# Performance work log

Hardware: AMD Instinct MI355X
Metric: run time of the kernel (lower is better)

## Reference

```python
import jax, jax.numpy as jnp
import numpy as np

D_MODEL = 512
D_STATE = 64
SEQ_LEN = 8192
BATCH = 8
LN_EPS = 1e-3  # keras LayerNormalization default epsilon
DELTA_MIN = 0.001
DELTA_MAX = 0.8 * (2.0 / D_STATE)  # default when use_hippo_init=True


def setup_inputs() -> dict:
    key = jax.random.key(0)
    ks = jax.random.split(key, 10)
    x = jax.random.normal(ks[0], (BATCH, SEQ_LEN, D_MODEL), dtype=jnp.float32)
    # Dense layers: glorot-uniform-ish init via scaled normal for simplicity
    def dense_w(k, fan_in, fan_out):
        lim = np.sqrt(6.0 / (fan_in + fan_out))
        return jax.random.uniform(k, (fan_in, fan_out), minval=-lim, maxval=lim, dtype=jnp.float32)
    W_in = dense_w(ks[1], D_MODEL, D_MODEL)
    b_in = jnp.zeros((D_MODEL,), jnp.float32)
    W_xs = dense_w(ks[2], D_MODEL, D_STATE)
    # HiPPO-LegS log init: A_log = log(n+1)
    A_log = jnp.log(jnp.arange(1, D_STATE + 1, dtype=jnp.float32))
    log_delta = jax.random.uniform(ks[3], (D_STATE,), minval=np.log(DELTA_MIN), maxval=np.log(DELTA_MAX), dtype=jnp.float32)
    B = jnp.ones((D_STATE,), jnp.float32)
    C = jax.random.normal(ks[4], (D_STATE,), dtype=jnp.float32)  # stddev=1.0
    D = jnp.ones((D_MODEL,), jnp.float32)
    W_so = dense_w(ks[5], D_STATE, D_MODEL)
    W_out = dense_w(ks[6], D_MODEL, D_MODEL)
    b_out = jnp.zeros((D_MODEL,), jnp.float32)
    ln_gamma = jnp.ones((D_MODEL,), jnp.float32)
    ln_beta = jnp.zeros((D_MODEL,), jnp.float32)
    return {
        "x": x, "ln_gamma": ln_gamma, "ln_beta": ln_beta,
        "W_in": W_in, "b_in": b_in, "W_xs": W_xs,
        "A_log": A_log, "log_delta": log_delta, "B": B, "C": C, "D": D,
        "W_so": W_so, "W_out": W_out, "b_out": b_out,
    }


def reference(x, ln_gamma, ln_beta, W_in, b_in, W_xs, A_log, log_delta, B, C, D, W_so, W_out, b_out):
    Bsz, L, dm = x.shape
    n_fft = 1 << int(np.ceil(np.log2(2 * L - 1)))
    residual = x
    # LayerNorm over last axis (keras default)
    mu = jnp.mean(x, axis=-1, keepdims=True)
    var = jnp.mean(jnp.square(x - mu), axis=-1, keepdims=True)
    xn = (x - mu) * jax.lax.rsqrt(var + LN_EPS) * ln_gamma + ln_beta
    z = xn @ W_in + b_in                       # (B, L, d_model)
    x_state = z @ W_xs                          # (B, L, d_state)
    # Diagonal SSM discretization (bilinear/Tustin)
    A = -jnp.exp(A_log)
    delta = jax.nn.softplus(log_delta)
    dA2 = delta * A / 2.0
    A_bar = (1.0 + dA2) / (1.0 - dA2)           # (d_state,)
    B_bar = delta / (1.0 - dA2) * B             # (d_state,)
    t = jnp.arange(L, dtype=jnp.float32)
    kernel = jnp.power(A_bar[None, :], t[:, None]) * B_bar[None, :]  # (L, d_state)
    # FFT convolution along time
    u_t = jnp.transpose(x_state, (0, 2, 1))     # (B, d_state, L)
    k_t = kernel.T                              # (d_state, L)
    u_f = jnp.fft.rfft(u_t, n=n_fft, axis=-1)
    k_f = jnp.fft.rfft(k_t, n=n_fft, axis=-1)
    y = jnp.fft.irfft(u_f * k_f[None, :, :], n=n_fft, axis=-1)[:, :, :L]
    y_state = jnp.transpose(y, (0, 2, 1))       # (B, L, d_state)
    y_state = y_state * C[None, None, :]
    y = y_state @ W_so                          # (B, L, d_model)
    y = y + D * z
    y = y @ W_out + b_out
    return y + residual
```

## Files before the change

### kernel.cpp

```cpp
#include <hip/hip_runtime.h>
#include <hip/hip_bf16.h>
#include <cstddef>
#include <cstdint>

#define DM 512
#define DS 64
#define L_SEQ 8192
#define NB 8
#define M_ROWS (NB * L_SEQ)
#define LN_EPS 1e-3f
#define NCHUNK 256
#define LCH 32

typedef __attribute__((ext_vector_type(8))) short short8;
typedef __attribute__((ext_vector_type(4))) float f32x4;
using bf16 = __hip_bfloat16;
using ushort_t = unsigned short;

__device__ __forceinline__ unsigned short f2bf(float f) {
    bf16 h = __float2bfloat16(f);
    return *reinterpret_cast<unsigned short*>(&h);
}

__device__ __forceinline__ int swzcol(int row, int col) {
    return (col & ~63) | (((((col >> 3) & 7) ^ (row & 7))) << 3) | (col & 7);
}

__device__ __forceinline__ size_t pkidx(int k, int n, int Kd32) {
    int n16 = n >> 4, fr = n & 15, kt = k >> 5, fq = (k >> 3) & 3, e = k & 7;
    return (((size_t)(n16 * Kd32 + kt) * 64 + fq * 16 + fr) << 3) + e;
}

__device__ __forceinline__ void gload_lds16(const void* g, void* l) {
    __builtin_amdgcn_global_load_lds(
        (const __attribute__((address_space(1))) void*)g,
        (__attribute__((address_space(3))) void*)l, 16, 0, 0);
}

template<int N> __device__ __forceinline__ void wait_vm() {
    static_assert(N == 0 || N == 2, "");
    if constexpr (N == 0) asm volatile("s_waitcnt vmcnt(0)" ::: "memory");
    else                  asm volatile("s_waitcnt vmcnt(2)" ::: "memory");
}

__device__ __forceinline__ void block_barrier() {
    asm volatile("" ::: "memory");
    __builtin_amdgcn_s_barrier();
    asm volatile("" ::: "memory");
}

__global__ __launch_bounds__(256) void prep(const float* __restrict__ W_so,
                                            const float* __restrict__ W_out,
                                            const float* __restrict__ W_in,
                                            const float* __restrict__ W_xs,
                                            const float* __restrict__ b_in,
                                            const float* __restrict__ b_out,
                                            const float* __restrict__ Dv,
                                            float* __restrict__ sWc2,
                                            float* __restrict__ sWc1,
                                            float* __restrict__ bc1,
                                            float* __restrict__ sWc3,
                                            float* __restrict__ bc2)
{
    int i = blockIdx.x * 256 + threadIdx.x;
    if (i < 32768) {
        int s = i >> 9, j = i & 511;
        float a = 0.f;
        for (int c = 0; c < 512; ++c) a += W_so[s * 512 + c] * W_out[c * 512 + j];
        sWc2[i] = a;
    } else if (i < 65536) {
        int idx = i - 32768; int k = idx >> 6, n = idx & 63;
        float a = 0.f;
        for (int c = 0; c < 512; ++c) a += W_in[k * 512 + c] * W_xs[c * 64 + n];
        sWc1[idx] = a;
    } else if (i < 65600) {
        int n = i - 65536;
        float a = 0.f;
        for (int c = 0; c < 512; ++c) a += b_in[c] * W_xs[c * 64 + n];
        bc1[n] = a;
    } else if (i < 327744) {
        int idx = i - 65600; int k = idx >> 9, j = idx & 511;
        float a = 0.f;
        for (int c = 0; c < 512; ++c) a += W_in[k * 512 + c] * Dv[c] * W_out[c * 512 + j];
        sWc3[idx] = a;
    } else if (i < 328256) {
        int j = i - 327744;
        float a = b_out[j];
        for (int c = 0; c < 512; ++c) a += b_in[c] * Dv[c] * W_out[c * 512 + j];
        bc2[j] = a;
    }
}

__global__ __launch_bounds__(256) void pack_all(const float* __restrict__ sWc3,
                                                const float* __restrict__ sWc1,
                                                const float* __restrict__ sWc2,
                                                ushort_t* __restrict__ Wc3Pk,
                                                ushort_t* __restrict__ Wc1Pk,
                                                ushort_t* __restrict__ Wc2Pk)
{
    int i = blockIdx.x * 256 + threadIdx.x;
    if (i < 262144) {
        int k = i >> 9, n = i & 511;
        Wc3Pk[pkidx(k, n, 16)] = f2bf(sWc3[i]);
    } else if (i < 294912) {
        int j = i - 262144; int k = j >> 6, n = j & 63;
        Wc1Pk[pkidx(k, n, 16)] = f2bf(sWc1[j]);
    } else if (i < 327680) {
        int j = i - 294912; int s = j >> 9, n = j & 511;
        Wc2Pk[pkidx(s, n, 2)] = f2bf(sWc2[j]);
    }
}

__global__ __launch_bounds__(256) void ln_xs(const float* __restrict__ x,
                                             const float* __restrict__ gamma,
                                             const float* __restrict__ beta,
                                             const ushort_t* __restrict__ Wc1Pk,
                                             const float* __restrict__ bc1,
                                             ushort_t* __restrict__ xn,
                                             float* __restrict__ xs)
{
    __shared__ ushort_t xt[16 * 512];
    const int tid = threadIdx.x;
    const int lane = tid & 63, w = tid >> 6;
    const int fr = lane & 15, fq = lane >> 4;
    const size_t row0 = (size_t)blockIdx.x * 16;

    const float4* g4 = (const float4*)gamma;
    const float4* b4 = (const float4*)beta;
    float4 g0 = g4[lane * 2], g1 = g4[lane * 2 + 1];
    float4 bb0 = b4[lane * 2], bb1 = b4[lane * 2 + 1];

    #pragma unroll
    for (int rr = 0; rr < 4; ++rr) {
        int r = w * 4 + rr;
        size_t row = row0 + r;
        const float4* xr = (const float4*)(x + row * DM);
        float4 v0 = xr[lane * 2], v1 = xr[lane * 2 + 1];
        float s  = v0.x + v0.y + v0.z + v0.w + v1.x + v1.y + v1.z + v1.w;
        float s2 = v0.x*v0.x + v0.y*v0.y + v0.z*v0.z + v0.w*v0.w
                 + v1.x*v1.x + v1.y*v1.y + v1.z*v1.z + v1.w*v1.w;
        #pragma unroll
        for (int off = 32; off > 0; off >>= 1) {
            s  += __shfl_xor(s,  off);
            s2 += __shfl_xor(s2, off);
        }
        float mu  = s * (1.0f / DM);
        float var = s2 * (1.0f / DM) - mu * mu;
        float rs  = rsqrtf(var + LN_EPS);
        short8 o;
        o[0] = (short)f2bf((v0.x - mu) * rs * g0.x + bb0.x);
        o[1] = (short)f2bf((v0.y - mu) * rs * g0.y + bb0.y);
        o[2] = (short)f2bf((v0.z - mu) * rs * g0.z + bb0.z);
        o[3] = (short)f2bf((v0.w - mu) * rs * g0.w + bb0.w);
        o[4] = (short)f2bf((v1.x - mu) * rs * g1.x + bb1.x);
        o[5] = (short)f2bf((v1.y - mu) * rs * g1.y + bb1.y);
        o[6] = (short)f2bf((v1.z - mu) * rs * g1.z + bb1.z);
        o[7] = (short)f2bf((v1.w - mu) * rs * g1.w + bb1.w);
        int g = (lane & 7) ^ ((int)row & 7);
        *(short8*)(xn + row * DM + (lane >> 3) * 64 + g * 8) = o;
        *(short8*)&xt[r * 512 + (lane >> 3) * 64 + g * 8] = o;
    }
    __syncthreads();

    f32x4 acc = (f32x4){0.f, 0.f, 0.f, 0.f};
    #pragma unroll
    for (int kt = 0; kt < 16; ++kt) {
        int seg = kt >> 1;
        int gk = ((kt & 1) * 4 + fq) ^ (fr & 7);
        short8 af = *(const short8*)&xt[fr * 512 + seg * 64 + gk * 8];
        short8 bf = *(const short8*)(Wc1Pk + (((size_t)(w * 16 + kt) * 64 + lane) << 3));
        acc = __builtin_amdgcn_mfma_f32_16x16x32_bf16(af, bf, acc, 0, 0, 0);
    }
    float bv = bc1[w * 16 + fr];
    #pragma unroll
    for (int r2 = 0; r2 < 4; ++r2)
        xs[(row0 + fq * 4 + r2) * DS + w * 16 + fr] = acc[r2] + bv;
}

__device__ __forceinline__ void store_out(float* C, size_t i, float v) { C[i] = v; }
__device__ __forceinline__ void store_out(bf16* C, size_t i, float v)  { C[i] = __float2bfloat16(v); }

template<int BN, int WR, int WC, typename OutT, bool DUAL, bool HB, bool HA, bool SWZO>
__global__ __launch_bounds__(512, 4) void gemm_bp(const ushort_t* __restrict__ A1,
                                                  const ushort_t* __restrict__ B1,
                                                  const ushort_t* __restrict__ A2,
                                                  const ushort_t* __restrict__ B2,
                                                  const float* __restrict__ bias,
                                                  const float* __restrict__ aux,
                                                  OutT* __restrict__ C,
                                                  int M, int N, int K2)
{
    constexpr int BM = 128;
    constexpr int MF = BM / (16 * WR), NF = BN / (16 * WC);
    static_assert(NF == 2, "b ping-pong arrays assume NF==2");
    __shared__ unsigned char LDS[3][BM * 128];

    const int tid = threadIdx.x;
    const int lane = tid & 63, w = tid >> 6;
    const int fr = lane & 15, fq = lane >> 4;
    const int wr = w % WR, wc = w / WR;

    const int ny = N / BN;
    const int per = (int)gridDim.x >> 3;
    const int lg = ((int)blockIdx.x & 7) * per + ((int)blockIdx.x >> 3);
    const size_t bm0 = (size_t)(lg / ny) * BM;
    const int bn0 = (lg % ny) * BN;
    const int nk = (DUAL ? 1 : 0) + K2 / 64;

    f32x4 acc[MF][NF];
    #pragma unroll
    for (int m = 0; m < MF; ++m)
        #pragma unroll
        for (int n = 0; n < NF; ++n)
            acc[m][n] = (f32x4){0.f, 0.f, 0.f, 0.f};

    auto stage = [&](int buf, int t) {
        #pragma unroll
        for (int j = 0; j < 2; ++j) {
            int r = j * 64 + (tid >> 3);
            const ushort_t* src;
            if constexpr (DUAL) {
                if (t == 0) src = A1 + (bm0 + r) * (size_t)64 + (tid & 7) * 8;
                else        src = A2 + (bm0 + r) * (size_t)512 + (size_t)(t - 1) * 64 + (tid & 7) * 8;
            } else {
                src = A2 + (bm0 + r) * (size_t)K2 + (size_t)t * 64 + (tid & 7) * 8;
            }
            gload_lds16(src, &LDS[buf][j * 8192 + w * 1024]);
        }
    };

    auto loadB = [&](short8 (&bb)[2][2], int t) {
        #pragma unroll
        for (int h = 0; h < 2; ++h)
            #pragma unroll
            for (int n = 0; n < NF; ++n) {
                int n16g = (bn0 + wc * (BN / WC) + n * 16) >> 4;
                const ushort_t* p;
                if constexpr (DUAL) {
                    if (t == 0) p = B1 + (((size_t)(n16g * 2 + h) * 64 + lane) << 3);
                    else        p = B2 + (((size_t)(n16g * 16 + (t - 1) * 2 + h) * 64 + lane) << 3);
                } else {
                    p = B2 + (((size_t)(n16g * (K2 / 32) + t * 2 + h) * 64 + lane) << 3);
                }
                bb[h][n] = *(const short8*)p;
            }
    };

    auto compute = [&](int buf, const short8 (&bb)[2][2]) {
        #pragma unroll
        for (int h = 0; h < 2; ++h) {
            short8 af[MF];
            #pragma unroll
            for (int m = 0; m < MF; ++m) {
                int row = wr * (BM / WR) + m * 16 + fr;
                int g = (h * 4 + fq) ^ (row & 7);
                af[m] = *(const short8*)&LDS[buf][row * 128 + g * 16];
            }
            #pragma unroll
            for (int m = 0; m < MF; ++m)
                #pragma unroll
                for (int n = 0; n < NF; ++n)
                    acc[m][n] = __builtin_amdgcn_mfma_f32_16x16x32_bf16(af[m], bb[h][n], acc[m][n], 0, 0, 0);
        }
    };

    short8 bX[2][2], bY[2][2];
    stage(0, 0);
    loadB(bX, 0);
    if (nk > 1) stage(1, 1);

    #define PHASE(T, BCUR, BNEXT)                                            \
        do {                                                                 \
            if ((T) + 1 < nk) wait_vm<2>(); else wait_vm<0>();               \
            block_barrier();                                                 \
            if ((T) + 1 < nk) loadB(BNEXT, (T) + 1);                         \
            if ((T) + 2 < nk) stage(((T) + 2) % 3, (T) + 2);                 \
            __builtin_amdgcn_sched_barrier(0);                               \
            compute((T) % 3, BCUR);                                          \
        } while (0)

    for (int t = 0; t < nk; t += 2) {
        PHASE(t, bX, bY);
        if (t + 1 < nk) PHASE(t + 1, bY, bX);
    }
    #undef PHASE

    #pragma unroll
    for (int n = 0; n < NF; ++n) {
        int coll = wc * (BN / WC) + n * 16 + fr;
        int colg = bn0 + coll;
        float bv = HB ? bias[colg] : 0.f;
        #pragma unroll
        for (int m = 0; m < MF; ++m) {
            int rowl = wr * (BM / WR) + m * 16 + fq * 4;
            #pragma unroll
            for (int r = 0; r < 4; ++r) {
                size_t row = bm0 + rowl + r;
                float v = acc[m][n][r] + bv;
                if constexpr (HA) v += aux[row * (size_t)N + colg];
                size_t oc = SWZO ? (size_t)swzcol(rowl + r, colg) : (size_t)colg;
                store_out(C, row * (size_t)N + oc, v);
            }
        }
    }
}

__device__ __forceinline__ void ssm_params(const float* A_log, const float* log_delta,
                                           const float* Bv, int n, float& Ab, float& Bb)
{
    float A  = -expf(A_log[n]);
    float dl = log1pf(expf(log_delta[n]));
    float dA2 = dl * A * 0.5f;
    float inv = 1.0f / (1.0f - dA2);
    Ab = (1.0f + dA2) * inv;
    Bb = dl * inv * Bv[n];
}

__global__ __launch_bounds__(64) void scan_pass1(const float* __restrict__ xs,
                                                 const float* __restrict__ A_log,
                                                 const float* __restrict__ log_delta,
                                                 const float* __restrict__ Bv,
                                                 float* __restrict__ carry)
{
    int b = blockIdx.x / NCHUNK;
    int c = blockIdx.x % NCHUNK;
    int n = threadIdx.x;
    float Ab, Bb;
    ssm_params(A_log, log_delta, Bv, n, Ab, Bb);
    size_t base = ((size_t)b * L_SEQ + (size_t)c * LCH) * DS + n;
    float h = 0.0f;
    for (int t = 0; t < LCH; ++t)
        h = Ab * h + Bb * xs[base + (size_t)t * DS];
    carry[((size_t)b * NCHUNK + c) * DS + n] = h;
}

__global__ __launch_bounds__(64) void scan_pass2(const float* __restrict__ A_log,
                                                 const float* __restrict__ log_delta,
                                                 const float* __restrict__ Bv,
                                                 const float* __restrict__ carry,
                                                 float* __restrict__ hin)
{
    int b = blockIdx.x;
    int n = threadIdx.x;
    float Ab, Bb;
    ssm_params(A_log, log_delta, Bv, n, Ab, Bb);
    float powA = powf(Ab, (float)LCH);
    float h = 0.0f;
    for (int c = 0; c < NCHUNK; ++c) {
        size_t idx = ((size_t)b * NCHUNK + c) * DS + n;
        hin[idx] = h;
        h = powA * h + carry[idx];
    }
}

__global__ __launch_bounds__(64) void scan_pass3(const float* __restrict__ xs,
                                                 const float* __restrict__ A_log,
                                                 const float* __restrict__ log_delta,
                                                 const float* __restrict__ Bv,
                                                 const float* __restrict__ Cv,
                                                 const float* __restrict__ hin,
                                                 ushort_t* __restrict__ ys)
{
    int b = blockIdx.x / NCHUNK;
    int c = blockIdx.x % NCHUNK;
    int n = threadIdx.x;
    float Ab, Bb;
    ssm_params(A_log, log_delta, Bv, n, Ab, Bb);
    float Cn = Cv[n];
    size_t base = ((size_t)b * L_SEQ + (size_t)c * LCH) * DS + n;
    size_t rowbase = ((size_t)b * L_SEQ + (size_t)c * LCH) * DS;
    float h = hin[((size_t)b * NCHUNK + c) * DS + n];
    for (int t = 0; t < LCH; ++t) {
        h = Ab * h + Bb * xs[base + (size_t)t * DS];
        int col = (((n >> 3) ^ (t & 7)) << 3) | (n & 7);
        ys[rowbase + (size_t)t * DS + col] = f2bf(Cn * h);
    }
}

extern "C" void kernel_launch(void* const* d_in, const int* in_sizes, int n_in,
                              void* d_out, int out_size, void* d_ws, size_t ws_size,
                              hipStream_t stream)
{
    const float* x         = (const float*)d_in[0];
    const float* ln_gamma  = (const float*)d_in[1];
    const float* ln_beta   = (const float*)d_in[2];
    const float* W_in      = (const float*)d_in[3];
    const float* b_in      = (const float*)d_in[4];
    const float* W_xs      = (const float*)d_in[5];
    const float* A_log     = (const float*)d_in[6];
    const float* log_delta = (const float*)d_in[7];
    const float* Bv        = (const float*)d_in[8];
    const float* Cv        = (const float*)d_in[9];
    const float* Dv        = (const float*)d_in[10];
    const float* W_so      = (const float*)d_in[11];
    const float* W_out     = (const float*)d_in[12];
    const float* b_out     = (const float*)d_in[13];
    float* out = (float*)d_out;

    const size_t M = M_ROWS;
    float*    xs_f   = (float*)d_ws;
    ushort_t* xn_b   = (ushort_t*)(xs_f + M * DS);
    ushort_t* ys_b   = xn_b + M * (size_t)DM;
    ushort_t* Wc3Pk  = ys_b + M * (size_t)DS;
    ushort_t* Wc1Pk  = Wc3Pk + (size_t)DM * DM;
    ushort_t* Wc2Pk  = Wc1Pk + (size_t)DM * DS;
    float*    sWc2   = (float*)(Wc2Pk + (size_t)DS * DM);
    float*    sWc1   = sWc2 + (size_t)DS * DM;
    float*    bc1    = sWc1 + (size_t)DM * DS;
    float*    sWc3   = bc1 + 64;
    float*    bc2    = sWc3 + (size_t)DM * DM;
    float*    carry  = bc2 + DM;
    float*    hin    = carry + NB * NCHUNK * DS;

    prep<<<dim3(1283), dim3(256), 0, stream>>>(W_so, W_out, W_in, W_xs, b_in, b_out, Dv,
                                               sWc2, sWc1, bc1, sWc3, bc2);
    pack_all<<<dim3(1280), dim3(256), 0, stream>>>(sWc3, sWc1, sWc2, Wc3Pk, Wc1Pk, Wc2Pk);
    ln_xs<<<dim3((unsigned)(M / 16)), dim3(256), 0, stream>>>(x, ln_gamma, ln_beta,
                                                              Wc1Pk, bc1, xn_b, xs_f);
    scan_pass1<<<dim3(NB * NCHUNK), dim3(64), 0, stream>>>(xs_f, A_log, log_delta, Bv, carry);
    scan_pass2<<<dim3(NB), dim3(64), 0, stream>>>(A_log, log_delta, Bv, carry, hin);
    scan_pass3<<<dim3(NB * NCHUNK), dim3(64), 0, stream>>>(xs_f, A_log, log_delta, Bv, Cv, hin, ys_b);
    gemm_bp<128, 2, 4, float, true, true, true, false>
        <<<dim3((M / 128) * (DM / 128)), dim3(512), 0, stream>>>(ys_b, Wc2Pk, xn_b, Wc3Pk,
                                                                 bc2, x, out, (int)M, DM, DM);
}
```

Baseline: 214.1 us.

## Fuse weight prep/pack, merge scan passes, replace final GEMM with full-row block kernel

Weight folding and bf16 packing now happen in a single kernel that writes packed weights directly, with no fp32 staging arrays. The sequential carry pass is removed: each chunk block recomputes its incoming state by looping over preceding chunk carries. The pipelined tiled dual GEMM is replaced by a kernel where each block loads a 64-row slab of xn into LDS once and eight waves each cover 64 output columns, with B fragments read directly from global. This cuts launches but adds redundant carry work (quadratic in chunk count) and drops the triple-buffered pipelining of the old GEMM.

After: 327.8 us. +53.1%, slower.

```diff
diff --git a/kernel.cpp b/kernel.cpp
--- a/kernel.cpp
+++ b/kernel.cpp
@@ -22,10 +22,6 @@
     return *reinterpret_cast<unsigned short*>(&h);
 }
 
-__device__ __forceinline__ int swzcol(int row, int col) {
-    return (col & ~63) | (((((col >> 3) & 7) ^ (row & 7))) << 3) | (col & 7);
-}
-
 __device__ __forceinline__ size_t pkidx(int k, int n, int Kd32) {
     int n16 = n >> 4, fr = n & 15, kt = k >> 5, fq = (k >> 3) & 3, e = k & 7;
     return (((size_t)(n16 * Kd32 + kt) * 64 + fq * 16 + fr) << 3) + e;
@@ -37,77 +33,45 @@
         (__attribute__((address_space(3))) void*)l, 16, 0, 0);
 }
 
-template<int N> __device__ __forceinline__ void wait_vm() {
-    static_assert(N == 0 || N == 2, "");
-    if constexpr (N == 0) asm volatile("s_waitcnt vmcnt(0)" ::: "memory");
-    else                  asm volatile("s_waitcnt vmcnt(2)" ::: "memory");
-}
-
-__device__ __forceinline__ void block_barrier() {
-    asm volatile("" ::: "memory");
-    __builtin_amdgcn_s_barrier();
-    asm volatile("" ::: "memory");
-}
-
-__global__ __launch_bounds__(256) void prep(const float* __restrict__ W_so,
-                                            const float* __restrict__ W_out,
-                                            const float* __restrict__ W_in,
-                                            const float* __restrict__ W_xs,
-                                            const float* __restrict__ b_in,
-                                            const float* __restrict__ b_out,
-                                            const float* __restrict__ Dv,
-                                            float* __restrict__ sWc2,
-                                            float* __restrict__ sWc1,
-                                            float* __restrict__ bc1,
-                                            float* __restrict__ sWc3,
-                                            float* __restrict__ bc2)
+__global__ __launch_bounds__(256) void wprep(const float* __restrict__ W_so,
+                                             const float* __restrict__ W_out,
+                                             const float* __restrict__ W_in,
+                                             const float* __restrict__ W_xs,
+                                             const float* __restrict__ b_in,
+                                             const float* __restrict__ b_out,
+                                             const float* __restrict__ Dv,
+                                             ushort_t* __restrict__ Wc3Pk,
+                                             ushort_t* __restrict__ Wc1Pk,
+                                             ushort_t* __restrict__ Wc2Pk,
+                                             float* __restrict__ bc1,
+                                             float* __restrict__ bc2)
 {
     int i = blockIdx.x * 256 + threadIdx.x;
-    if (i < 32768) {
-        int s = i >> 9, j = i & 511;
+    if (i < 262144) {
+        int k = i >> 9, n = i & 511;
         float a = 0.f;
-        for (int c = 0; c < 512; ++c) a += W_so[s * 512 + c] * W_out[c * 512 + j];
-        sWc2[i] = a;
-    } else if (i < 65536) {
-        int idx = i - 32768; int k = idx >> 6, n = idx & 63;
+        for (int c = 0; c < 512; ++c) a += W_in[k * 512 + c] * Dv[c] * W_out[c * 512 + n];
+        Wc3Pk[pkidx(k, n, 16)] = f2bf(a);
+    } else if (i < 294912) {
+        int j = i - 262144; int k = j >> 6, n = j & 63;
         float a = 0.f;
         for (int c = 0; c < 512; ++c) a += W_in[k * 512 + c] * W_xs[c * 64 + n];
-        sWc1[idx] = a;
-    } else if (i < 65600) {
-        int n = i - 65536;
+        Wc1Pk[pkidx(k, n, 16)] = f2bf(a);
+    } else if (i < 327680) {
+        int j = i - 294912; int s = j >> 9, n = j & 511;
+        float a = 0.f;
+        for (int c = 0; c < 512; ++c) a += W_so[s * 512 + c] * W_out[c * 512 + n];
+        Wc2Pk[pkidx(s, n, 2)] = f2bf(a);
+    } else if (i < 328192) {
+        int n = i - 327680;
+        float a = b_out[n];
+        for (int c = 0; c < 512; ++c) a += b_in[c] * Dv[c] * W_out[c * 512 + n];
+        bc2[n] = a;
+    } else if (i < 328256) {
+        int n = i - 328192;
         float a = 0.f;
         for (int c = 0; c < 512; ++c) a += b_in[c] * W_xs[c * 64 + n];
         bc1[n] = a;
-    } else if (i < 327744) {
-        int idx = i - 65600; int k = idx >> 9, j = idx & 511;
-        float a = 0.f;
-        for (int c = 0; c < 512; ++c) a += W_in[k * 512 + c] * Dv[c] * W_out[c * 512 + j];
-        sWc3[idx] = a;
-    } else if (i < 328256) {
-        int j = i - 327744;
-        float a = b_out[j];
-        for (int c = 0; c < 512; ++c) a += b_in[c] * Dv[c] * W_out[c * 512 + j];
-        bc2[j] = a;
-    }
-}
-
-__global__ __launch_bounds__(256) void pack_all(const float* __restrict__ sWc3,
-                                                const float* __restrict__ sWc1,
-                                                const float* __restrict__ sWc2,
-                                                ushort_t* __restrict__ Wc3Pk,
-                                                ushort_t* __restrict__ Wc1Pk,
-                                                ushort_t* __restrict__ Wc2Pk)
-{
-    int i = blockIdx.x * 256 + threadIdx.x;
-    if (i < 262144) {
-        int k = i >> 9, n = i & 511;
-        Wc3Pk[pkidx(k, n, 16)] = f2bf(sWc3[i]);
-    } else if (i < 294912) {
-        int j = i - 262144; int k = j >> 6, n = j & 63;
-        Wc1Pk[pkidx(k, n, 16)] = f2bf(sWc1[j]);
-    } else if (i < 327680) {
-        int j = i - 294912; int s = j >> 9, n = j & 511;
-        Wc2Pk[pkidx(s, n, 2)] = f2bf(sWc2[j]);
     }
 }
 
@@ -177,134 +141,6 @@
         xs[(row0 + fq * 4 + r2) * DS + w * 16 + fr] = acc[r2] + bv;
 }
 
-__device__ __forceinline__ void store_out(float* C, size_t i, float v) { C[i] = v; }
-__device__ __forceinline__ void store_out(bf16* C, size_t i, float v)  { C[i] = __float2bfloat16(v); }
-
-template<int BN, int WR, int WC, typename OutT, bool DUAL, bool HB, bool HA, bool SWZO>
-__global__ __launch_bounds__(512, 4) void gemm_bp(const ushort_t* __restrict__ A1,
-                                                  const ushort_t* __restrict__ B1,
-                                                  const ushort_t* __restrict__ A2,
-                                                  const ushort_t* __restrict__ B2,
-                                                  const float* __restrict__ bias,
-                                                  const float* __restrict__ aux,
-                                                  OutT* __restrict__ C,
-                                                  int M, int N, int K2)
-{
-    constexpr int BM = 128;
-    constexpr int MF = BM / (16 * WR), NF = BN / (16 * WC);
-    static_assert(NF == 2, "b ping-pong arrays assume NF==2");
-    __shared__ unsigned char LDS[3][BM * 128];
-
-    const int tid = threadIdx.x;
-    const int lane = tid & 63, w = tid >> 6;
-    const int fr = lane & 15, fq = lane >> 4;
-    const int wr = w % WR, wc = w / WR;
-
-    const int ny = N / BN;
-    const int per = (int)gridDim.x >> 3;
-    const int lg = ((int)blockIdx.x & 7) * per + ((int)blockIdx.x >> 3);
-    const size_t bm0 = (size_t)(lg / ny) * BM;
-    const int bn0 = (lg % ny) * BN;
-    const int nk = (DUAL ? 1 : 0) + K2 / 64;
-
-    f32x4 acc[MF][NF];
-    #pragma unroll
-    for (int m = 0; m < MF; ++m)
-        #pragma unroll
-        for (int n = 0; n < NF; ++n)
-            acc[m][n] = (f32x4){0.f, 0.f, 0.f, 0.f};
-
-    auto stage = [&](int buf, int t) {
-        #pragma unroll
-        for (int j = 0; j < 2; ++j) {
-            int r = j * 64 + (tid >> 3);
-            const ushort_t* src;
-            if constexpr (DUAL) {
-                if (t == 0) src = A1 + (bm0 + r) * (size_t)64 + (tid & 7) * 8;
-                else        src = A2 + (bm0 + r) * (size_t)512 + (size_t)(t - 1) * 64 + (tid & 7) * 8;
-            } else {
-                src = A2 + (bm0 + r) * (size_t)K2 + (size_t)t * 64 + (tid & 7) * 8;
-            }
-            gload_lds16(src, &LDS[buf][j * 8192 + w * 1024]);
-        }
-    };
-
-    auto loadB = [&](short8 (&bb)[2][2], int t) {
-        #pragma unroll
-        for (int h = 0; h < 2; ++h)
-            #pragma unroll
-            for (int n = 0; n < NF; ++n) {
-                int n16g = (bn0 + wc * (BN / WC) + n * 16) >> 4;
-                const ushort_t* p;
-                if constexpr (DUAL) {
-                    if (t == 0) p = B1 + (((size_t)(n16g * 2 + h) * 64 + lane) << 3);
-                    else        p = B2 + (((size_t)(n16g * 16 + (t - 1) * 2 + h) * 64 + lane) << 3);
-                } else {
-                    p = B2 + (((size_t)(n16g * (K2 / 32) + t * 2 + h) * 64 + lane) << 3);
-                }
-                bb[h][n] = *(const short8*)p;
-            }
-    };
-
-    auto compute = [&](int buf, const short8 (&bb)[2][2]) {
-        #pragma unroll
-        for (int h = 0; h < 2; ++h) {
-            short8 af[MF];
-            #pragma unroll
-            for (int m = 0; m < MF; ++m) {
-                int row = wr * (BM / WR) + m * 16 + fr;
-                int g = (h * 4 + fq) ^ (row & 7);
-                af[m] = *(const short8*)&LDS[buf][row * 128 + g * 16];
-            }
-            #pragma unroll
-            for (int m = 0; m < MF; ++m)
-                #pragma unroll
-                for (int n = 0; n < NF; ++n)
-                    acc[m][n] = __builtin_amdgcn_mfma_f32_16x16x32_bf16(af[m], bb[h][n], acc[m][n], 0, 0, 0);
-        }
-    };
-
-    short8 bX[2][2], bY[2][2];
-    stage(0, 0);
-    loadB(bX, 0);
-    if (nk > 1) stage(1, 1);
-
-    #define PHASE(T, BCUR, BNEXT)                                            \
-        do {                                                                 \
-            if ((T) + 1 < nk) wait_vm<2>(); else wait_vm<0>();               \
-            block_barrier();                                                 \
-            if ((T) + 1 < nk) loadB(BNEXT, (T) + 1);                         \
-            if ((T) + 2 < nk) stage(((T) + 2) % 3, (T) + 2);                 \
-            __builtin_amdgcn_sched_barrier(0);                               \
-            compute((T) % 3, BCUR);                                          \
-        } while (0)
-
-    for (int t = 0; t < nk; t += 2) {
-        PHASE(t, bX, bY);
-        if (t + 1 < nk) PHASE(t + 1, bY, bX);
-    }
-    #undef PHASE
-
-    #pragma unroll
-    for (int n = 0; n < NF; ++n) {
-        int coll = wc * (BN / WC) + n * 16 + fr;
-        int colg = bn0 + coll;
-        float bv = HB ? bias[colg] : 0.f;
-        #pragma unroll
-        for (int m = 0; m < MF; ++m) {
-            int rowl = wr * (BM / WR) + m * 16 + fq * 4;
-            #pragma unroll
-            for (int r = 0; r < 4; ++r) {
-                size_t row = bm0 + rowl + r;
-                float v = acc[m][n][r] + bv;
-                if constexpr (HA) v += aux[row * (size_t)N + colg];
-                size_t oc = SWZO ? (size_t)swzcol(rowl + r, colg) : (size_t)colg;
-                store_out(C, row * (size_t)N + oc, v);
-            }
-        }
-    }
-}
-
 __device__ __forceinline__ void ssm_params(const float* A_log, const float* log_delta,
                                            const float* Bv, int n, float& Ab, float& Bb)
 {
@@ -334,32 +170,13 @@
     carry[((size_t)b * NCHUNK + c) * DS + n] = h;
 }
 
-__global__ __launch_bounds__(64) void scan_pass2(const float* __restrict__ A_log,
-                                                 const float* __restrict__ log_delta,
-                                                 const float* __restrict__ Bv,
-                                                 const float* __restrict__ carry,
-                                                 float* __restrict__ hin)
-{
-    int b = blockIdx.x;
-    int n = threadIdx.x;
-    float Ab, Bb;
-    ssm_params(A_log, log_delta, Bv, n, Ab, Bb);
-    float powA = powf(Ab, (float)LCH);
-    float h = 0.0f;
-    for (int c = 0; c < NCHUNK; ++c) {
-        size_t idx = ((size_t)b * NCHUNK + c) * DS + n;
-        hin[idx] = h;
-        h = powA * h + carry[idx];
-    }
-}
-
-__global__ __launch_bounds__(64) void scan_pass3(const float* __restrict__ xs,
-                                                 const float* __restrict__ A_log,
-                                                 const float* __restrict__ log_delta,
-                                                 const float* __restrict__ Bv,
-                                                 const float* __restrict__ Cv,
-                                                 const float* __restrict__ hin,
-                                                 ushort_t* __restrict__ ys)
+__global__ __launch_bounds__(64) void scan_pass23(const float* __restrict__ xs,
+                                                  const float* __restrict__ A_log,
+                                                  const float* __restrict__ log_delta,
+                                                  const float* __restrict__ Bv,
+                                                  const float* __restrict__ Cv,
+                                                  const float* __restrict__ carry,
+                                                  ushort_t* __restrict__ ys)
 {
     int b = blockIdx.x / NCHUNK;
     int c = blockIdx.x % NCHUNK;
@@ -367,13 +184,106 @@
     float Ab, Bb;
     ssm_params(A_log, log_delta, Bv, n, Ab, Bb);
     float Cn = Cv[n];
+    float powL = powf(Ab, (float)LCH);
+    float h = 0.0f;
+    for (int cp = 0; cp < c; ++cp)
+        h = powL * h + carry[((size_t)b * NCHUNK + cp) * DS + n];
     size_t base = ((size_t)b * L_SEQ + (size_t)c * LCH) * DS + n;
     size_t rowbase = ((size_t)b * L_SEQ + (size_t)c * LCH) * DS;
-    float h = hin[((size_t)b * NCHUNK + c) * DS + n];
     for (int t = 0; t < LCH; ++t) {
         h = Ab * h + Bb * xs[base + (size_t)t * DS];
         int col = (((n >> 3) ^ (t & 7)) << 3) | (n & 7);
         ys[rowbase + (size_t)t * DS + col] = f2bf(Cn * h);
+    }
+}
+
+__global__ __launch_bounds__(512, 4) void gd_fused(const ushort_t* __restrict__ ys,
+                                                   const ushort_t* __restrict__ xn,
+                                                   const ushort_t* __restrict__ Wc2Pk,
+                                                   const ushort_t* __restrict__ Wc3Pk,
+                                                   const float* __restrict__ bc2,
+                                                   const float* __restrict__ x,
+                                                   float* __restrict__ out)
+{
+    __shared__ ushort_t Xs[64 * 512];
+    const int tid = threadIdx.x;
+    const int lane = tid & 63, w = tid >> 6;
+    const int fr = lane & 15, fq = lane >> 4;
+    const size_t bm0 = (size_t)blockIdx.x * 64;
+    const int cn0 = w * 64;
+    const int n16g0 = w * 4;
+
+    short8 ay[2][4], by[2][4];
+    #pragma unroll
+    for (int kt = 0; kt < 2; ++kt)
+        #pragma unroll
+        for (int m = 0; m < 4; ++m) {
+            int row = m * 16 + fr;
+            int g = (kt * 4 + fq) ^ (row & 7);
+            ay[kt][m] = *(const short8*)(ys + (bm0 + row) * (size_t)64 + g * 8);
+        }
+    #pragma unroll
+    for (int kt = 0; kt < 2; ++kt)
+        #pragma unroll
+        for (int n = 0; n < 4; ++n)
+            by[kt][n] = *(const short8*)(Wc2Pk + (((size_t)((n16g0 + n) * 2 + kt) * 64 + lane) << 3));
+
+    #pragma unroll
+    for (int j = 0; j < 8; ++j) {
+        int row = j * 8 + w;
+        gload_lds16(xn + (bm0 + row) * (size_t)512 + lane * 8,
+                    &Xs[(size_t)j * 4096 + w * 512]);
+    }
+
+    f32x4 acc[4][4];
+    #pragma unroll
+    for (int m = 0; m < 4; ++m)
+        #pragma unroll
+        for (int n = 0; n < 4; ++n)
+            acc[m][n] = (f32x4){0.f, 0.f, 0.f, 0.f};
+    #pragma unroll
+    for (int kt = 0; kt < 2; ++kt)
+        #pragma unroll
+        for (int m = 0; m < 4; ++m)
+            #pragma unroll
+            for (int n = 0; n < 4; ++n)
+                acc[m][n] = __builtin_amdgcn_mfma_f32_16x16x32_bf16(ay[kt][m], by[kt][n], acc[m][n], 0, 0, 0);
+
+    __syncthreads();
+
+    #pragma unroll
+    for (int kt = 0; kt < 16; ++kt) {
+        short8 af[4], bf[4];
+        #pragma unroll
+        for (int m = 0; m < 4; ++m) {
+            int row = m * 16 + fr;
+            int G = kt * 4 + fq;
+            int gi = (G & ~7) | ((G & 7) ^ (row & 7));
+            af[m] = *(const short8*)&Xs[row * 512 + gi * 8];
+        }
+        #pragma unroll
+        for (int n = 0; n < 4; ++n)
+            bf[n] = *(const short8*)(Wc3Pk + (((size_t)((n16g0 + n) * 16 + kt) * 64 + lane) << 3));
+        #pragma unroll
+        for (int m = 0; m < 4; ++m)
+            #pragma unroll
+            for (int n = 0; n < 4; ++n)
+                acc[m][n] = __builtin_amdgcn_mfma_f32_16x16x32_bf16(af[m], bf[n], acc[m][n], 0, 0, 0);
+    }
+
+    #pragma unroll
+    for (int n = 0; n < 4; ++n) {
+        int colg = cn0 + n * 16 + fr;
+        float bv = bc2[colg];
+        #pragma unroll
+        for (int m = 0; m < 4; ++m) {
+            size_t row = bm0 + m * 16 + fq * 4;
+            #pragma unroll
+            for (int r = 0; r < 4; ++r) {
+                size_t idx = (row + r) * (size_t)DM + colg;
+                out[idx] = acc[m][n][r] + bv + x[idx];
+            }
+        }
     }
 }
 
@@ -404,23 +314,17 @@
     ushort_t* Wc3Pk  = ys_b + M * (size_t)DS;
     ushort_t* Wc1Pk  = Wc3Pk + (size_t)DM * DM;
     ushort_t* Wc2Pk  = Wc1Pk + (size_t)DM * DS;
-    float*    sWc2   = (float*)(Wc2Pk + (size_t)DS * DM);
-    float*    sWc1   = sWc2 + (size_t)DS * DM;
-    float*    bc1    = sWc1 + (size_t)DM * DS;
-    float*    sWc3   = bc1 + 64;
-    float*    bc2    = sWc3 + (size_t)DM * DM;
+    float*    bc1    = (float*)(Wc2Pk + (size_t)DS * DM);
+    float*    bc2    = bc1 + 64;
     float*    carry  = bc2 + DM;
-    float*    hin    = carry + NB * NCHUNK * DS;
-
-    prep<<<dim3(1283), dim3(256), 0, stream>>>(W_so, W_out, W_in, W_xs, b_in, b_out, Dv,
-                                               sWc2, sWc1, bc1, sWc3, bc2);
-    pack_all<<<dim3(1280), dim3(256), 0, stream>>>(sWc3, sWc1, sWc2, Wc3Pk, Wc1Pk, Wc2Pk);
+
+    wprep<<<dim3(1283), dim3(256), 0, stream>>>(W_so, W_out, W_in, W_xs, b_in, b_out, Dv,
+                                                Wc3Pk, Wc1Pk, Wc2Pk, bc1, bc2);
     ln_xs<<<dim3((unsigned)(M / 16)), dim3(256), 0, stream>>>(x, ln_gamma, ln_beta,
                                                               Wc1Pk, bc1, xn_b, xs_f);
     scan_pass1<<<dim3(NB * NCHUNK), dim3(64), 0, stream>>>(xs_f, A_log, log_delta, Bv, carry);
-    scan_pass2<<<dim3(NB), dim3(64), 0, stream>>>(A_log, log_delta, Bv, carry, hin);
-    scan_pass3<<<dim3(NB * NCHUNK), dim3(64), 0, stream>>>(xs_f, A_log, log_delta, Bv, Cv, hin, ys_b);
-    gemm_bp<128, 2, 4, float, true, true, true, false>
-        <<<dim3((M / 128) * (DM / 128)), dim3(512), 0, stream>>>(ys_b, Wc2Pk, xn_b, Wc3Pk,
-                                                                 bc2, x, out, (int)M, DM, DM);
-}
+    scan_pass23<<<dim3(NB * NCHUNK), dim3(64), 0, stream>>>(xs_f, A_log, log_delta, Bv, Cv,
+                                                            carry, ys_b);
+    gd_fused<<<dim3((unsigned)(M / 64)), dim3(512), 0, stream>>>(ys_b, xn_b, Wc2Pk, Wc3Pk,
+                                                                 bc2, x, out);
+}
```
